# Performance work log

Hardware: AMD Instinct MI355X
Metric: run time of the kernel (lower is better)

## Reference

```python
import jax, jax.numpy as jnp
import numpy as np

EMBED_DIM = 256
NUM_HEADS = 8
HEAD_DIM = EMBED_DIM // NUM_HEADS
SCALE = HEAD_DIM ** -0.5  # note: scale uses head_dim even though attention is over full D
EPS = 1e-12  # torch F.normalize eps


def setup_inputs() -> dict:
    key = jax.random.key(0)
    k1, k2, k3 = jax.random.split(key, 3)
    B, Nq, Nk, D = 4, 4096, 4096, EMBED_DIM
    return {
        "query": jax.random.normal(k1, (B, Nq, D), dtype=jnp.float32),
        "key": jax.random.normal(k2, (B, Nk, D), dtype=jnp.float32),
        "value": jax.random.normal(k3, (B, Nk, D), dtype=jnp.float32),
    }


def _l2_normalize(x):
    # matches torch.nn.functional.normalize(x, dim=-1): x / max(||x||, eps)
    n = jnp.linalg.norm(x, axis=-1, keepdims=True)
    return x / jnp.maximum(n, EPS)


def reference(query, key, value):
    q = _l2_normalize(query)          # (B, Nq, D)
    k = _l2_normalize(key)            # (B, Nk, D)
    scores = jnp.einsum("bqd,bkd->bqk", q, k) * SCALE  # (B, Nq, Nk) cosine sims
    attn = jax.nn.softmax(scores, axis=-1)
    return jnp.einsum("bqk,bkd->bqd", attn, value)     # (B, Nq, D)
```

## Files before the change

kernel.cpp:

```cpp
#include <hip/hip_runtime.h>


#define NQ 4096
#define DIM 256
#define NROWS 16384
#define BM 64
#define BN 64
#define KSPLIT 2
#define NITER 32
#define PSTRIDE 68

typedef __attribute__((ext_vector_type(8))) short bf16x8;
typedef __attribute__((ext_vector_type(4))) float f32x4;
typedef __attribute__((ext_vector_type(16))) float f32x16;

__device__ __forceinline__ unsigned short f2bf(float f) {
  unsigned int u = __float_as_uint(f);
  u += 0x7fffu + ((u >> 16) & 1u);
  return (unsigned short)(u >> 16);
}

__device__ __forceinline__ unsigned int pack2bf(float a, float b) {
  unsigned int ua = __float_as_uint(a) + 0x8000u;
  unsigned int ub = __float_as_uint(b) + 0x8000u;
  return __builtin_amdgcn_perm(ub, ua, 0x07060302u);
}

__device__ __forceinline__ void gload16(const void* g, void* l) {
  __builtin_amdgcn_global_load_lds(
      (const __attribute__((address_space(1))) unsigned int*)g,
      (__attribute__((address_space(3))) unsigned int*)l, 16, 0, 0);
}

__global__ __launch_bounds__(256) void prep(
    const float* __restrict__ Q, const float* __restrict__ K,
    const float* __restrict__ V,
    unsigned short* __restrict__ Qrm, unsigned short* __restrict__ Kfm,
    unsigned short* __restrict__ Vfm)
{
  __shared__ unsigned short vt[16 * 264];
  const int blk = blockIdx.x, tid = threadIdx.x;
  if (blk < 8192) {
    const int wave = tid >> 6, lane = tid & 63;
    const int r = blk * 4 + wave;
    const bool isQ = r < NROWS;
    const int R = isQ ? r : r - NROWS;
    float4 v = *(const float4*)((isQ ? Q : K) + (size_t)R * DIM + lane * 4);
    float ss = v.x*v.x + v.y*v.y + v.z*v.z + v.w*v.w;
    #pragma unroll
    for (int off = 1; off < 64; off <<= 1) ss += __shfl_xor(ss, off, 64);
    float scale = 1.0f / fmaxf(sqrtf(ss), 1e-12f);
    if (isQ) scale *= (0.17677669529663687f * 1.4426950408889634f);
    ushort4 o;
    o.x = f2bf(v.x*scale); o.y = f2bf(v.y*scale);
    o.z = f2bf(v.z*scale); o.w = f2bf(v.w*scale);
    if (isQ) {
      *(ushort4*)(Qrm + (size_t)R * DIM + lane * 4) = o;
    } else {
      const int kt = R >> 6, n = R & 63;
      const int c = lane >> 1, j0 = 4 * (lane & 1);
      *(ushort4*)(Kfm + ((size_t)(kt*32 + c)*64 + n)*8 + j0) = o;
    }
  } else {
    const int NS = blk - 8192;
    #pragma unroll
    for (int i = 0; i < 4; i++) {
      const int e = tid + 256*i;
      const int nl = e >> 6, d = (e & 63) * 4;
      float4 v = *(const float4*)(V + ((size_t)NS*16 + nl)*DIM + d);
      ushort4 o;
      o.x = f2bf(v.x); o.y = f2bf(v.y); o.z = f2bf(v.z); o.w = f2bf(v.w);
      *(ushort4*)(vt + nl*264 + d) = o;
    }
    __syncthreads();
    #pragma unroll
    for (int i = 0; i < 2; i++) {
      const int ch = tid + 256*i;
      const int db = ch >> 6, ln = ch & 63;
      const int row0 = (ln >> 5) * 8, dd = db*32 + (ln & 31);
      ushort4 a, b;
      a.x = vt[(row0+0)*264 + dd]; a.y = vt[(row0+1)*264 + dd];
      a.z = vt[(row0+2)*264 + dd]; a.w = vt[(row0+3)*264 + dd];
      b.x = vt[(row0+4)*264 + dd]; b.y = vt[(row0+5)*264 + dd];
      b.z = vt[(row0+6)*264 + dd]; b.w = vt[(row0+7)*264 + dd];
      size_t base = ((size_t)(NS*8 + db)*64 + ln)*8;
      *(ushort4*)(Vfm + base)     = a;
      *(ushort4*)(Vfm + base + 4) = b;
    }
  }
}

__global__ __launch_bounds__(256, 2) void attn(
    const unsigned short* __restrict__ Qrm,
    const unsigned short* __restrict__ Kfm,
    const unsigned short* __restrict__ Vfm,
    float* __restrict__ Opart, float* __restrict__ lpart)
{
  __shared__ unsigned short Klds[32 * 64 * 8];
  __shared__ unsigned short Plds[BM * PSTRIDE];

  const int tid = threadIdx.x, wave = tid >> 6, lane = tid & 63;
  const int l15 = lane & 15, l4 = lane >> 4;
  const int blk = blockIdx.x;
  const int g = blk & 7, qt = blk >> 3;
  const int b = g >> 1, ks = g & 1;
  const int Rq0 = b*NQ + qt*BM;
  const int n0base = b*NQ + ks*(NQ/KSPLIT);
  const int mi = wave & 1, ni = wave >> 1;

  bf16x8 qf[2][8];
  #pragma unroll
  for (int mt = 0; mt < 2; mt++) {
    const unsigned short* qrow = Qrm + (size_t)(Rq0 + mi*32 + mt*16 + l15) * DIM + l4*8;
    #pragma unroll
    for (int kg = 0; kg < 8; kg++)
      qf[mt][kg] = *(const bf16x8*)(qrow + kg*32);
  }

  f32x16 oacc[2][2] = {};
  float lacc[2] = {};

  auto stage = [&](int kt) {
    const unsigned short* src = Kfm + (size_t)((n0base + kt*BN) >> 6) * (32*64*8);
    #pragma unroll
    for (int jj = 0; jj < 4; jj++) {
      const int c = wave*8 + jj*2;
      gload16(src + (size_t)c*512 + lane*8,       Klds + (size_t)c*512);
      gload16(src + (size_t)(c+1)*512 + lane*8,   Klds + (size_t)(c+1)*512);
    }
  };

  stage(0);

  for (int kt = 0; kt < NITER; kt++) {
    __syncthreads();

    f32x4 sacc[2][2] = {};
    #pragma unroll
    for (int kg = 0; kg < 8; kg++) {
      bf16x8 kf[2];
      #pragma unroll
      for (int nt = 0; nt < 2; nt++) {
        const int nrow = ni*32 + nt*16 + l15;
        const int c = kg*4 + l4;
        kf[nt] = *(const bf16x8*)(Klds + ((size_t)(c*64 + nrow))*8);
      }
      #pragma unroll
      for (int nt = 0; nt < 2; nt++)
        #pragma unroll
        for (int mt = 0; mt < 2; mt++)
          sacc[nt][mt] = __builtin_amdgcn_mfma_f32_16x16x32_bf16(
              kf[nt], qf[mt][kg], sacc[nt][mt], 0, 0, 0);
    }

    #pragma unroll
    for (int nt = 0; nt < 2; nt++)
      #pragma unroll
      for (int mt = 0; mt < 2; mt++) {
        float p0 = __builtin_amdgcn_exp2f(sacc[nt][mt][0]);
        float p1 = __builtin_amdgcn_exp2f(sacc[nt][mt][1]);
        float p2 = __builtin_amdgcn_exp2f(sacc[nt][mt][2]);
        float p3 = __builtin_amdgcn_exp2f(sacc[nt][mt][3]);
        lacc[mt] += (p0 + p1) + (p2 + p3);
        uint2 pk;
        pk.x = pack2bf(p0, p1);
        pk.y = pack2bf(p2, p3);
        const int m = mi*32 + mt*16 + l15;
        const int n = ni*32 + nt*16 + 4*l4;
        *(uint2*)(Plds + m*PSTRIDE + n) = pk;
      }

    __syncthreads();

    if (kt + 1 < NITER) stage(kt + 1);

    const int NB0 = (n0base + kt*BN) >> 4;
    #pragma unroll
    for (int kstep = 0; kstep < 4; kstep++) {
      bf16x8 pf[2], vf[2];
      #pragma unroll
      for (int mt2 = 0; mt2 < 2; mt2++)
        pf[mt2] = *(const bf16x8*)(Plds + (mt2*32 + (lane & 31))*PSTRIDE
                                   + kstep*16 + 8*(lane >> 5));
      #pragma unroll
      for (int dt = 0; dt < 2; dt++) {
        const int db = wave*2 + dt;
        vf[dt] = *(const bf16x8*)(Vfm + ((size_t)((NB0 + kstep)*8 + db)*64 + lane)*8);
      }
      #pragma unroll
      for (int mt2 = 0; mt2 < 2; mt2++)
        #pragma unroll
        for (int dt = 0; dt < 2; dt++)
          oacc[mt2][dt] = __builtin_amdgcn_mfma_f32_32x32x16_bf16(
              pf[mt2], vf[dt], oacc[mt2][dt], 0, 0, 0);
    }
  }

  #pragma unroll
  for (int mt = 0; mt < 2; mt++) {
    float s = lacc[mt];
    s += __shfl_xor(s, 16, 64);
    s += __shfl_xor(s, 32, 64);
    if (l4 == 0)
      lpart[(size_t)(ks*2 + ni)*NROWS + Rq0 + mi*32 + mt*16 + l15] = s;
  }

  #pragma unroll
  for (int mt2 = 0; mt2 < 2; mt2++)
    #pragma unroll
    for (int dt = 0; dt < 2; dt++)
      #pragma unroll
      for (int reg = 0; reg < 16; reg++) {
        const int m = mt2*32 + 4*(lane >> 5) + (reg & 3) + 8*(reg >> 2);
        const int d = wave*64 + dt*32 + (lane & 31);
        Opart[((size_t)(ks*NROWS + Rq0 + m))*DIM + d] = oacc[mt2][dt][reg];
      }
}

__global__ __launch_bounds__(256) void combine(
    const float* __restrict__ Opart, const float* __restrict__ lpart,
    float* __restrict__ out)
{
  const size_t idx = (size_t)blockIdx.x*256 + threadIdx.x;
  const size_t e = idx*4;
  const int R = (int)(e >> 8);
  float4 a = *(const float4*)(Opart + e);
  float4 c = *(const float4*)(Opart + (size_t)NROWS*DIM + e);
  float ls = lpart[R] + lpart[NROWS + R] + lpart[2*NROWS + R] + lpart[3*NROWS + R];
  float inv = 1.0f / ls;
  float4 o;
  o.x = (a.x + c.x)*inv; o.y = (a.y + c.y)*inv;
  o.z = (a.z + c.z)*inv; o.w = (a.w + c.w)*inv;
  *(float4*)(out + e) = o;
}

extern "C" void kernel_launch(void* const* d_in, const int* in_sizes, int n_in,
                              void* d_out, int out_size, void* d_ws, size_t ws_size,
                              hipStream_t stream) {
  const float* Q = (const float*)d_in[0];
  const float* K = (const float*)d_in[1];
  const float* V = (const float*)d_in[2];
  char* ws = (char*)d_ws;
  unsigned short* Qrm = (unsigned short*)(ws);
  unsigned short* Kfm = (unsigned short*)(ws + 8388608);
  unsigned short* Vfm = (unsigned short*)(ws + 16777216);
  float* Opart = (float*)(ws + 25165824);
  float* lpart = (float*)(ws + 58720256);

  prep<<<9216, 256, 0, stream>>>(Q, K, V, Qrm, Kfm, Vfm);
  attn<<<512, 256, 0, stream>>>(Qrm, Kfm, Vfm, Opart, lpart);
  combine<<<4096, 256, 0, stream>>>(Opart, lpart, (float*)d_out);
}
```

Measured before the change: 180.9 us.

## Double-buffer K tiles, use 8 waves per block, swizzle P in LDS

The attention kernel goes from 4 to 8 waves per block. Each wave now handles a 16-key slice for the QK^T step and a 32x64 output slice for PV. K tiles are double-buffered in LDS so the next tile's async load overlaps the current compute, and the P tile uses an XOR-swizzled layout in place of padding. The K prep is also rewritten so each block writes the fragment layout coalesced through LDS, and combine now sums 8 partial row sums. This costs an extra barrier per iteration, more LDS per block and more lpart traffic, in exchange for more latency hiding.

Result: slower. 248.1 us (+37.1%).

```diff
diff --git a/kernel.cpp b/kernel.cpp
--- a/kernel.cpp
+++ b/kernel.cpp
@@ -8,7 +8,6 @@
 #define BN 64
 #define KSPLIT 2
 #define NITER 32
-#define PSTRIDE 68
 
 typedef __attribute__((ext_vector_type(8))) short bf16x8;
 typedef __attribute__((ext_vector_type(4))) float f32x4;
@@ -38,31 +37,46 @@
     unsigned short* __restrict__ Qrm, unsigned short* __restrict__ Kfm,
     unsigned short* __restrict__ Vfm)
 {
-  __shared__ unsigned short vt[16 * 264];
+  __shared__ unsigned short vt[64 * 264];
   const int blk = blockIdx.x, tid = threadIdx.x;
-  if (blk < 8192) {
-    const int wave = tid >> 6, lane = tid & 63;
-    const int r = blk * 4 + wave;
-    const bool isQ = r < NROWS;
-    const int R = isQ ? r : r - NROWS;
-    float4 v = *(const float4*)((isQ ? Q : K) + (size_t)R * DIM + lane * 4);
+  const int wave = tid >> 6, lane = tid & 63;
+  if (blk < 4096) {
+    const int R = blk * 4 + wave;
+    float4 v = *(const float4*)(Q + (size_t)R * DIM + lane * 4);
     float ss = v.x*v.x + v.y*v.y + v.z*v.z + v.w*v.w;
     #pragma unroll
     for (int off = 1; off < 64; off <<= 1) ss += __shfl_xor(ss, off, 64);
-    float scale = 1.0f / fmaxf(sqrtf(ss), 1e-12f);
-    if (isQ) scale *= (0.17677669529663687f * 1.4426950408889634f);
+    float scale = (0.17677669529663687f * 1.4426950408889634f)
+                  / fmaxf(sqrtf(ss), 1e-12f);
     ushort4 o;
     o.x = f2bf(v.x*scale); o.y = f2bf(v.y*scale);
     o.z = f2bf(v.z*scale); o.w = f2bf(v.w*scale);
-    if (isQ) {
-      *(ushort4*)(Qrm + (size_t)R * DIM + lane * 4) = o;
-    } else {
-      const int kt = R >> 6, n = R & 63;
-      const int c = lane >> 1, j0 = 4 * (lane & 1);
-      *(ushort4*)(Kfm + ((size_t)(kt*32 + c)*64 + n)*8 + j0) = o;
+    *(ushort4*)(Qrm + (size_t)R * DIM + lane * 4) = o;
+  } else if (blk < 4352) {
+    const int kt = blk - 4096;
+    #pragma unroll
+    for (int i = 0; i < 16; i++) {
+      const int n = i*4 + wave;
+      float4 v = *(const float4*)(K + ((size_t)kt*64 + n) * DIM + lane * 4);
+      float ss = v.x*v.x + v.y*v.y + v.z*v.z + v.w*v.w;
+      #pragma unroll
+      for (int off = 1; off < 64; off <<= 1) ss += __shfl_xor(ss, off, 64);
+      float scale = 1.0f / fmaxf(sqrtf(ss), 1e-12f);
+      ushort4 o;
+      o.x = f2bf(v.x*scale); o.y = f2bf(v.y*scale);
+      o.z = f2bf(v.z*scale); o.w = f2bf(v.w*scale);
+      *(ushort4*)(vt + n*264 + lane*4) = o;
+    }
+    __syncthreads();
+    #pragma unroll
+    for (int s = 0; s < 8; s++) {
+      const int ch = tid + 256*s;
+      const int c = ch >> 6, n = ch & 63;
+      bf16x8 val = *(const bf16x8*)(vt + n*264 + c*8);
+      *(bf16x8*)(Kfm + (size_t)kt*16384 + (size_t)ch*8) = val;
     }
   } else {
-    const int NS = blk - 8192;
+    const int NS = blk - 4352;
     #pragma unroll
     for (int i = 0; i < 4; i++) {
       const int e = tid + 256*i;
@@ -90,110 +104,95 @@
   }
 }
 
-__global__ __launch_bounds__(256, 2) void attn(
+__global__ __launch_bounds__(512, 4) void attn(
     const unsigned short* __restrict__ Qrm,
     const unsigned short* __restrict__ Kfm,
     const unsigned short* __restrict__ Vfm,
     float* __restrict__ Opart, float* __restrict__ lpart)
 {
-  __shared__ unsigned short Klds[32 * 64 * 8];
-  __shared__ unsigned short Plds[BM * PSTRIDE];
+  __shared__ unsigned short Klds[2][32 * 64 * 8];
+  __shared__ unsigned short Plds[64 * 64];
 
   const int tid = threadIdx.x, wave = tid >> 6, lane = tid & 63;
   const int l15 = lane & 15, l4 = lane >> 4;
+  const int l31 = lane & 31, l5 = lane >> 5;
   const int blk = blockIdx.x;
   const int g = blk & 7, qt = blk >> 3;
   const int b = g >> 1, ks = g & 1;
   const int Rq0 = b*NQ + qt*BM;
   const int n0base = b*NQ + ks*(NQ/KSPLIT);
-  const int mi = wave & 1, ni = wave >> 1;
+  const int mi = wave >> 2, ni = wave & 3;
+  const int mh = wave & 1,  dh = wave >> 1;
 
   bf16x8 qf[2][8];
   #pragma unroll
   for (int mt = 0; mt < 2; mt++) {
-    const unsigned short* qrow = Qrm + (size_t)(Rq0 + mi*32 + mt*16 + l15) * DIM + l4*8;
+    const unsigned short* qrow = Qrm + (size_t)(Rq0 + mi*32 + mt*16 + l15)*DIM + l4*8;
     #pragma unroll
     for (int kg = 0; kg < 8; kg++)
       qf[mt][kg] = *(const bf16x8*)(qrow + kg*32);
   }
 
-  f32x16 oacc[2][2] = {};
+  f32x16 oacc[2] = {};
   float lacc[2] = {};
 
-  auto stage = [&](int kt) {
+  auto stage = [&](int kt, int sel) {
     const unsigned short* src = Kfm + (size_t)((n0base + kt*BN) >> 6) * (32*64*8);
+    unsigned short* dst = &Klds[sel][0];
     #pragma unroll
     for (int jj = 0; jj < 4; jj++) {
-      const int c = wave*8 + jj*2;
-      gload16(src + (size_t)c*512 + lane*8,       Klds + (size_t)c*512);
-      gload16(src + (size_t)(c+1)*512 + lane*8,   Klds + (size_t)(c+1)*512);
+      const int c = wave*4 + jj;
+      gload16(src + (size_t)c*512 + lane*8, dst + (size_t)c*512);
     }
   };
 
-  stage(0);
+  stage(0, 0);
+  __syncthreads();
 
   for (int kt = 0; kt < NITER; kt++) {
-    __syncthreads();
-
-    f32x4 sacc[2][2] = {};
+    if (kt + 1 < NITER) stage(kt + 1, (kt + 1) & 1);
+
+    const unsigned short* kb = &Klds[kt & 1][0];
+    f32x4 sacc[2] = {};
     #pragma unroll
     for (int kg = 0; kg < 8; kg++) {
-      bf16x8 kf[2];
-      #pragma unroll
-      for (int nt = 0; nt < 2; nt++) {
-        const int nrow = ni*32 + nt*16 + l15;
-        const int c = kg*4 + l4;
-        kf[nt] = *(const bf16x8*)(Klds + ((size_t)(c*64 + nrow))*8);
-      }
-      #pragma unroll
-      for (int nt = 0; nt < 2; nt++)
-        #pragma unroll
-        for (int mt = 0; mt < 2; mt++)
-          sacc[nt][mt] = __builtin_amdgcn_mfma_f32_16x16x32_bf16(
-              kf[nt], qf[mt][kg], sacc[nt][mt], 0, 0, 0);
-    }
-
-    #pragma unroll
-    for (int nt = 0; nt < 2; nt++)
-      #pragma unroll
-      for (int mt = 0; mt < 2; mt++) {
-        float p0 = __builtin_amdgcn_exp2f(sacc[nt][mt][0]);
-        float p1 = __builtin_amdgcn_exp2f(sacc[nt][mt][1]);
-        float p2 = __builtin_amdgcn_exp2f(sacc[nt][mt][2]);
-        float p3 = __builtin_amdgcn_exp2f(sacc[nt][mt][3]);
-        lacc[mt] += (p0 + p1) + (p2 + p3);
-        uint2 pk;
-        pk.x = pack2bf(p0, p1);
-        pk.y = pack2bf(p2, p3);
-        const int m = mi*32 + mt*16 + l15;
-        const int n = ni*32 + nt*16 + 4*l4;
-        *(uint2*)(Plds + m*PSTRIDE + n) = pk;
-      }
-
-    __syncthreads();
-
-    if (kt + 1 < NITER) stage(kt + 1);
+      bf16x8 kf = *(const bf16x8*)(kb + ((size_t)((kg*4 + l4)*64 + ni*16 + l15))*8);
+      sacc[0] = __builtin_amdgcn_mfma_f32_16x16x32_bf16(kf, qf[0][kg], sacc[0], 0, 0, 0);
+      sacc[1] = __builtin_amdgcn_mfma_f32_16x16x32_bf16(kf, qf[1][kg], sacc[1], 0, 0, 0);
+    }
+
+    #pragma unroll
+    for (int mt = 0; mt < 2; mt++) {
+      float p0 = __builtin_amdgcn_exp2f(sacc[mt][0]);
+      float p1 = __builtin_amdgcn_exp2f(sacc[mt][1]);
+      float p2 = __builtin_amdgcn_exp2f(sacc[mt][2]);
+      float p3 = __builtin_amdgcn_exp2f(sacc[mt][3]);
+      lacc[mt] += (p0 + p1) + (p2 + p3);
+      uint2 pk;
+      pk.x = pack2bf(p0, p1);
+      pk.y = pack2bf(p2, p3);
+      const int m = mi*32 + mt*16 + l15;
+      const int c = ni*2 + (l4 >> 1);
+      *(uint2*)(Plds + m*64 + ((c ^ (m & 7)) << 3) + (l4 & 1)*4) = pk;
+    }
+
+    __syncthreads();
 
     const int NB0 = (n0base + kt*BN) >> 4;
     #pragma unroll
     for (int kstep = 0; kstep < 4; kstep++) {
-      bf16x8 pf[2], vf[2];
-      #pragma unroll
-      for (int mt2 = 0; mt2 < 2; mt2++)
-        pf[mt2] = *(const bf16x8*)(Plds + (mt2*32 + (lane & 31))*PSTRIDE
-                                   + kstep*16 + 8*(lane >> 5));
+      const int m = mh*32 + l31;
+      const int c = kstep*2 + l5;
+      bf16x8 pf = *(const bf16x8*)(Plds + m*64 + ((c ^ (m & 7)) << 3));
       #pragma unroll
       for (int dt = 0; dt < 2; dt++) {
-        const int db = wave*2 + dt;
-        vf[dt] = *(const bf16x8*)(Vfm + ((size_t)((NB0 + kstep)*8 + db)*64 + lane)*8);
+        bf16x8 vf = *(const bf16x8*)(Vfm +
+            ((size_t)((NB0 + kstep)*8 + dh*2 + dt)*64 + lane)*8);
+        oacc[dt] = __builtin_amdgcn_mfma_f32_32x32x16_bf16(pf, vf, oacc[dt], 0, 0, 0);
       }
-      #pragma unroll
-      for (int mt2 = 0; mt2 < 2; mt2++)
-        #pragma unroll
-        for (int dt = 0; dt < 2; dt++)
-          oacc[mt2][dt] = __builtin_amdgcn_mfma_f32_32x32x16_bf16(
-              pf[mt2], vf[dt], oacc[mt2][dt], 0, 0, 0);
-    }
+    }
+
+    __syncthreads();
   }
 
   #pragma unroll
@@ -202,19 +201,17 @@
     s += __shfl_xor(s, 16, 64);
     s += __shfl_xor(s, 32, 64);
     if (l4 == 0)
-      lpart[(size_t)(ks*2 + ni)*NROWS + Rq0 + mi*32 + mt*16 + l15] = s;
-  }
-
-  #pragma unroll
-  for (int mt2 = 0; mt2 < 2; mt2++)
-    #pragma unroll
-    for (int dt = 0; dt < 2; dt++)
-      #pragma unroll
-      for (int reg = 0; reg < 16; reg++) {
-        const int m = mt2*32 + 4*(lane >> 5) + (reg & 3) + 8*(reg >> 2);
-        const int d = wave*64 + dt*32 + (lane & 31);
-        Opart[((size_t)(ks*NROWS + Rq0 + m))*DIM + d] = oacc[mt2][dt][reg];
-      }
+      lpart[(size_t)(ks*4 + ni)*NROWS + Rq0 + mi*32 + mt*16 + l15] = s;
+  }
+
+  #pragma unroll
+  for (int dt = 0; dt < 2; dt++)
+    #pragma unroll
+    for (int reg = 0; reg < 16; reg++) {
+      const int m = mh*32 + 4*l5 + (reg & 3) + 8*(reg >> 2);
+      const int d = dh*64 + dt*32 + l31;
+      Opart[((size_t)(ks*NROWS + Rq0 + m))*DIM + d] = oacc[dt][reg];
+    }
 }
 
 __global__ __launch_bounds__(256) void combine(
@@ -226,7 +223,9 @@
   const int R = (int)(e >> 8);
   float4 a = *(const float4*)(Opart + e);
   float4 c = *(const float4*)(Opart + (size_t)NROWS*DIM + e);
-  float ls = lpart[R] + lpart[NROWS + R] + lpart[2*NROWS + R] + lpart[3*NROWS + R];
+  float ls = 0.f;
+  #pragma unroll
+  for (int s = 0; s < 8; s++) ls += lpart[(size_t)s*NROWS + R];
   float inv = 1.0f / ls;
   float4 o;
   o.x = (a.x + c.x)*inv; o.y = (a.y + c.y)*inv;
@@ -247,7 +246,7 @@
   float* Opart = (float*)(ws + 25165824);
   float* lpart = (float*)(ws + 58720256);
 
-  prep<<<9216, 256, 0, stream>>>(Q, K, V, Qrm, Kfm, Vfm);
-  attn<<<512, 256, 0, stream>>>(Qrm, Kfm, Vfm, Opart, lpart);
+  prep<<<5376, 256, 0, stream>>>(Q, K, V, Qrm, Kfm, Vfm);
+  attn<<<512, 512, 0, stream>>>(Qrm, Kfm, Vfm, Opart, lpart);
   combine<<<4096, 256, 0, stream>>>(Opart, lpart, (float*)d_out);
 }
```

## Double-buffer K tiles in LDS and coalesce K prep writes via LDS transpose

Applied to the files above, without the earlier changes.

The attention kernel now keeps two K tiles in LDS. It issues the next tile's global-to-LDS load at the start of each iteration, so the load overlaps both the QK and PV phases. The mid-iteration barrier now waits only on LDS counters, which keeps those global loads in flight. The prep kernel now normalizes 64 K rows per block into LDS and writes the fragment-major K layout as contiguous 16-byte chunks, replacing scattered 8-byte stores. The cost is doubled K LDS use, which still has to fit two blocks per CU, plus an extra LDS round-trip in prep.

Measured after the change: 188.1 us. +4.0%, slower.

```diff
diff --git a/kernel.cpp b/kernel.cpp
--- a/kernel.cpp
+++ b/kernel.cpp
@@ -32,37 +32,57 @@
       (__attribute__((address_space(3))) unsigned int*)l, 16, 0, 0);
 }
 
+__device__ __forceinline__ void barrier_lds_only() {
+  asm volatile("s_waitcnt lgkmcnt(0)" ::: "memory");
+  __builtin_amdgcn_s_barrier();
+}
+
 __global__ __launch_bounds__(256) void prep(
     const float* __restrict__ Q, const float* __restrict__ K,
     const float* __restrict__ V,
     unsigned short* __restrict__ Qrm, unsigned short* __restrict__ Kfm,
     unsigned short* __restrict__ Vfm)
 {
-  __shared__ unsigned short vt[16 * 264];
+  __shared__ unsigned short vt[64 * 264];
   const int blk = blockIdx.x, tid = threadIdx.x;
-  if (blk < 8192) {
-    const int wave = tid >> 6, lane = tid & 63;
-    const int r = blk * 4 + wave;
-    const bool isQ = r < NROWS;
-    const int R = isQ ? r : r - NROWS;
-    float4 v = *(const float4*)((isQ ? Q : K) + (size_t)R * DIM + lane * 4);
+  const int wave = tid >> 6, lane = tid & 63;
+  if (blk < 4096) {
+    const int R = blk * 4 + wave;
+    float4 v = *(const float4*)(Q + (size_t)R * DIM + lane * 4);
     float ss = v.x*v.x + v.y*v.y + v.z*v.z + v.w*v.w;
     #pragma unroll
     for (int off = 1; off < 64; off <<= 1) ss += __shfl_xor(ss, off, 64);
-    float scale = 1.0f / fmaxf(sqrtf(ss), 1e-12f);
-    if (isQ) scale *= (0.17677669529663687f * 1.4426950408889634f);
+    float scale = (0.17677669529663687f * 1.4426950408889634f)
+                  / fmaxf(sqrtf(ss), 1e-12f);
     ushort4 o;
     o.x = f2bf(v.x*scale); o.y = f2bf(v.y*scale);
     o.z = f2bf(v.z*scale); o.w = f2bf(v.w*scale);
-    if (isQ) {
-      *(ushort4*)(Qrm + (size_t)R * DIM + lane * 4) = o;
-    } else {
-      const int kt = R >> 6, n = R & 63;
-      const int c = lane >> 1, j0 = 4 * (lane & 1);
-      *(ushort4*)(Kfm + ((size_t)(kt*32 + c)*64 + n)*8 + j0) = o;
+    *(ushort4*)(Qrm + (size_t)R * DIM + lane * 4) = o;
+  } else if (blk < 4352) {
+    const int kt = blk - 4096;
+    #pragma unroll
+    for (int i = 0; i < 16; i++) {
+      const int n = i*4 + wave;
+      float4 v = *(const float4*)(K + ((size_t)kt*64 + n) * DIM + lane * 4);
+      float ss = v.x*v.x + v.y*v.y + v.z*v.z + v.w*v.w;
+      #pragma unroll
+      for (int off = 1; off < 64; off <<= 1) ss += __shfl_xor(ss, off, 64);
+      float scale = 1.0f / fmaxf(sqrtf(ss), 1e-12f);
+      ushort4 o;
+      o.x = f2bf(v.x*scale); o.y = f2bf(v.y*scale);
+      o.z = f2bf(v.z*scale); o.w = f2bf(v.w*scale);
+      *(ushort4*)(vt + n*264 + lane*4) = o;
+    }
+    __syncthreads();
+    #pragma unroll
+    for (int s = 0; s < 8; s++) {
+      const int ch = tid + 256*s;
+      const int c = ch >> 6, n = ch & 63;
+      bf16x8 val = *(const bf16x8*)(vt + n*264 + c*8);
+      *(bf16x8*)(Kfm + (size_t)kt*16384 + (size_t)ch*8) = val;
     }
   } else {
-    const int NS = blk - 8192;
+    const int NS = blk - 4352;
     #pragma unroll
     for (int i = 0; i < 4; i++) {
       const int e = tid + 256*i;
@@ -96,7 +116,7 @@
     const unsigned short* __restrict__ Vfm,
     float* __restrict__ Opart, float* __restrict__ lpart)
 {
-  __shared__ unsigned short Klds[32 * 64 * 8];
+  __shared__ unsigned short Klds[2][32 * 64 * 8];
   __shared__ unsigned short Plds[BM * PSTRIDE];
 
   const int tid = threadIdx.x, wave = tid >> 6, lane = tid & 63;
@@ -120,21 +140,24 @@
   f32x16 oacc[2][2] = {};
   float lacc[2] = {};
 
-  auto stage = [&](int kt) {
+  auto stage = [&](int kt, int sel) {
     const unsigned short* src = Kfm + (size_t)((n0base + kt*BN) >> 6) * (32*64*8);
+    unsigned short* dst = &Klds[sel][0];
     #pragma unroll
     for (int jj = 0; jj < 4; jj++) {
       const int c = wave*8 + jj*2;
-      gload16(src + (size_t)c*512 + lane*8,       Klds + (size_t)c*512);
-      gload16(src + (size_t)(c+1)*512 + lane*8,   Klds + (size_t)(c+1)*512);
+      gload16(src + (size_t)c*512 + lane*8,     dst + (size_t)c*512);
+      gload16(src + (size_t)(c+1)*512 + lane*8, dst + (size_t)(c+1)*512);
     }
   };
 
-  stage(0);
+  stage(0, 0);
+  __syncthreads();
 
   for (int kt = 0; kt < NITER; kt++) {
-    __syncthreads();
-
+    if (kt + 1 < NITER) stage(kt + 1, (kt + 1) & 1);
+
+    const unsigned short* kb = &Klds[kt & 1][0];
     f32x4 sacc[2][2] = {};
     #pragma unroll
     for (int kg = 0; kg < 8; kg++) {
@@ -143,7 +166,7 @@
       for (int nt = 0; nt < 2; nt++) {
         const int nrow = ni*32 + nt*16 + l15;
         const int c = kg*4 + l4;
-        kf[nt] = *(const bf16x8*)(Klds + ((size_t)(c*64 + nrow))*8);
+        kf[nt] = *(const bf16x8*)(kb + ((size_t)(c*64 + nrow))*8);
       }
       #pragma unroll
       for (int nt = 0; nt < 2; nt++)
@@ -170,9 +193,7 @@
         *(uint2*)(Plds + m*PSTRIDE + n) = pk;
       }
 
-    __syncthreads();
-
-    if (kt + 1 < NITER) stage(kt + 1);
+    barrier_lds_only();
 
     const int NB0 = (n0base + kt*BN) >> 4;
     #pragma unroll
@@ -194,6 +215,8 @@
           oacc[mt2][dt] = __builtin_amdgcn_mfma_f32_32x32x16_bf16(
               pf[mt2], vf[dt], oacc[mt2][dt], 0, 0, 0);
     }
+
+    __syncthreads();
   }
 
   #pragma unroll
@@ -247,7 +270,7 @@
   float* Opart = (float*)(ws + 25165824);
   float* lpart = (float*)(ws + 58720256);
 
-  prep<<<9216, 256, 0, stream>>>(Q, K, V, Qrm, Kfm, Vfm);
+  prep<<<5376, 256, 0, stream>>>(Q, K, V, Qrm, Kfm, Vfm);
   attn<<<512, 256, 0, stream>>>(Qrm, Kfm, Vfm, Opart, lpart);
   combine<<<4096, 256, 0, stream>>>(Opart, lpart, (float*)d_out);
 }
```
